# Optimization experiments

Hardware: AMD Instinct MI355X
Metric: run time of the kernel (lower is better)

Reference implementation:

```python
import jax, jax.numpy as jnp
import numpy as np

B, S, H = 128, 512, 512  # batch, seq_len, hidden_units; feature dim is 2H = 1024
D = 2 * H


def setup_inputs() -> dict:
    key = jax.random.key(0)
    ks = jax.random.split(key, 8)
    scale = 1.0 / np.sqrt(D)
    return {
        "h_dec": jax.random.normal(ks[0], (1, B, H), jnp.float32),
        "c_dec": jax.random.normal(ks[1], (1, B, H), jnp.float32),
        "encoder_output": jax.random.normal(ks[2], (B, S, D), jnp.float32),
        "x_padding_masks": jnp.ones((B, S), jnp.float32),
        "coverage_vector": jax.random.uniform(ks[3], (B, S), jnp.float32),
        "Wh_w": jax.random.normal(ks[4], (D, D), jnp.float32) * scale,
        "Ws_w": jax.random.normal(ks[5], (D, D), jnp.float32) * scale,
        "Ws_b": jax.random.normal(ks[6], (D,), jnp.float32) * scale,
        "v_w": jax.random.normal(ks[7], (D,), jnp.float32) * scale,
        "wc_w": jax.random.normal(jax.random.fold_in(key, 99), (D,), jnp.float32) * scale,
    }


def reference(h_dec, c_dec, encoder_output, x_padding_masks, coverage_vector,
              Wh_w, Ws_w, Ws_b, v_w, wc_w):
    # s_t: concat(h, c) -> (B, 2H)
    s_t = jnp.concatenate([h_dec[0], c_dec[0]], axis=-1)  # (B, D)
    enc_feat = jnp.einsum('bsd,ed->bse', encoder_output, Wh_w)       # Wh(enc)
    dec_feat = s_t @ Ws_w.T + Ws_b                                    # (B, D)
    cov_feat = coverage_vector[:, :, None] * wc_w[None, None, :]      # w_c(cov)
    att_inputs = enc_feat + dec_feat[:, None, :] + cov_feat           # (B, S, D)
    score = jnp.tanh(att_inputs) @ v_w                                # (B, S)
    aw = jax.nn.softmax(score, axis=1) * x_padding_masks              # masked softmax
    aw = aw / jnp.sum(aw, axis=1, keepdims=True)                      # renormalize
    context_vector = jnp.einsum('bs,bsd->bd', aw, encoder_output)     # (B, D)
    new_coverage = coverage_vector + aw
    return context_vector, aw, new_coverage
```

## Files before the change

### kernel.cpp

```cpp
#include <hip/hip_runtime.h>
#include <hip/hip_bf16.h>
#include <cstdint>
#include <cstddef>


typedef __attribute__((ext_vector_type(8))) short bf16x8;
typedef __attribute__((ext_vector_type(4))) float f32x4;

#define GLOBAL_AS(p) ((const __attribute__((address_space(1))) unsigned int*)(p))
#define LDS_AS(p)    ((__attribute__((address_space(3))) unsigned int*)(p))

__device__ __forceinline__ short f2bf(float f) {
    union { float f; uint32_t u; } v; v.f = f;
    uint32_t u = v.u + 0x7fffu + ((v.u >> 16) & 1u);
    return (short)(u >> 16);
}

__device__ __forceinline__ float bf2f(short s) {
    union { uint32_t u; float f; } v; v.u = ((uint32_t)(uint16_t)s) << 16;
    return v.f;
}

__device__ __forceinline__ bf16x8 cvt8(float4 a, float4 b) {
    bf16x8 r;
    r[0] = f2bf(a.x); r[1] = f2bf(a.y); r[2] = f2bf(a.z); r[3] = f2bf(a.w);
    r[4] = f2bf(b.x); r[5] = f2bf(b.y); r[6] = f2bf(b.z); r[7] = f2bf(b.w);
    return r;
}

__device__ __forceinline__ float fast_tanh(float x) {
    x = fminf(10.f, fmaxf(-10.f, x));
    float e = __expf(2.f * x);
    return (e - 1.f) / (e + 1.f);
}

__global__ __launch_bounds__(256) void cvt_all(
    const float* __restrict__ enc, const float* __restrict__ Wh,
    short* __restrict__ enc_bf, short* __restrict__ Wh_bf)
{
    size_t i = ((size_t)blockIdx.x * 256 + threadIdx.x) * 8;
    const float* src; short* dst; size_t off;
    const size_t NE = 67108864;
    if (i < NE) { src = enc; dst = enc_bf; off = i; }
    else        { src = Wh;  dst = Wh_bf;  off = i - NE; }
    float4 a = *(const float4*)(src + off);
    float4 b = *(const float4*)(src + off + 4);
    *(bf16x8*)(dst + off) = cvt8(a, b);
}

__global__ void cvt_f32_bf16(const float* __restrict__ src, short* __restrict__ dst, int n) {
    int i = (blockIdx.x * 256 + threadIdx.x) * 4;
    if (i < n) {
        float4 f = *(const float4*)(src + i);
        short4 o;
        o.x = f2bf(f.x); o.y = f2bf(f.y); o.z = f2bf(f.z); o.w = f2bf(f.w);
        *(short4*)(dst + i) = o;
    }
}

__global__ __launch_bounds__(256) void dec_gemm_sk(
    const float* __restrict__ hd, const float* __restrict__ cd,
    const float* __restrict__ Ws, float* __restrict__ dec_part)
{
    __shared__ __align__(16) short As[128 * 40];
    __shared__ __align__(16) short Bs[128 * 40];
    const int t = threadIdx.x;
    const int bx = blockIdx.x & 7;
    const int kc = blockIdx.x >> 3;
    const int wv = t >> 6, lane = t & 63, q = lane >> 4, c = lane & 15;
    const int wm = wv & 1, wn = wv >> 1;
    const int ar = t >> 1, ah = t & 1;

    const float* abase = ((kc < 2) ? hd : cd) + (size_t)ar * 512 + (kc & 1) * 256 + ah * 16;
    const float* bbase = Ws + ((size_t)(bx * 128 + ar)) * 1024 + kc * 256 + ah * 16;
    short* awr = &As[ar * 40 + ah * 16];
    short* bwr = &Bs[ar * 40 + ah * 16];

    f32x4 acc[4][4];
#pragma unroll
    for (int i = 0; i < 4; ++i)
#pragma unroll
        for (int j = 0; j < 4; ++j) acc[i][j] = (f32x4){0.f, 0.f, 0.f, 0.f};

    for (int k0 = 0; k0 < 256; k0 += 32) {
        const float4* ap = (const float4*)(abase + k0);
        const float4* bp = (const float4*)(bbase + k0);
        float4 a0 = ap[0], a1 = ap[1], a2 = ap[2], a3 = ap[3];
        float4 b0 = bp[0], b1 = bp[1], b2 = bp[2], b3 = bp[3];
        *(bf16x8*)awr = cvt8(a0, a1);
        *(bf16x8*)(awr + 8) = cvt8(a2, a3);
        *(bf16x8*)bwr = cvt8(b0, b1);
        *(bf16x8*)(bwr + 8) = cvt8(b2, b3);
        __syncthreads();
        bf16x8 af[4], bf[4];
#pragma unroll
        for (int i = 0; i < 4; ++i) af[i] = *(const bf16x8*)&As[(wm * 64 + i * 16 + c) * 40 + q * 8];
#pragma unroll
        for (int j = 0; j < 4; ++j) bf[j] = *(const bf16x8*)&Bs[(wn * 64 + j * 16 + c) * 40 + q * 8];
#pragma unroll
        for (int i = 0; i < 4; ++i)
#pragma unroll
            for (int j = 0; j < 4; ++j)
                acc[i][j] = __builtin_amdgcn_mfma_f32_16x16x32_bf16(af[i], bf[j], acc[i][j], 0, 0, 0);
        __syncthreads();
    }

    const int n0 = bx * 128 + wn * 64;
    float* dp = dec_part + (size_t)kc * 131072;
#pragma unroll
    for (int i = 0; i < 4; ++i)
#pragma unroll
        for (int rr = 0; rr < 4; ++rr) {
            int bidx = wm * 64 + i * 16 + q * 4 + rr;
#pragma unroll
            for (int j = 0; j < 4; ++j)
                dp[(size_t)bidx * 1024 + n0 + j * 16 + c] = acc[i][j][rr];
        }
}

__global__ __launch_bounds__(256) void attn_score_gemm4(
    const short* __restrict__ encb, const short* __restrict__ Whb,
    const float* __restrict__ dec_part, const float* __restrict__ Wsb,
    const float* __restrict__ cov,
    const float* __restrict__ wc_w, const float* __restrict__ v_w,
    float* __restrict__ p_part)
{
    __shared__ __align__(16) short As[2][128 * 32];
    __shared__ __align__(16) short Bs[2][128 * 32];
    const int t = threadIdx.x;
    const int lin = blockIdx.x;
    const int xcd = lin & 7;
    const int kk  = lin >> 3;
    const int bx  = kk & 7;
    const int by  = xcd * 64 + (kk >> 3);
    const int b   = by >> 2;
    const int s0  = (by & 3) * 128;

    const int wv = t >> 6, lane = t & 63, q = lane >> 4, c = lane & 15;
    const int wm = wv & 1, wn = wv >> 1;

    const int srow = wv * 16 + (lane >> 2);
    const int gg = (lane & 3) ^ ((srow ^ (srow >> 2)) & 3);
    const short* ag0 = encb + ((size_t)(by * 128 + srow)) * 1024 + gg * 8;
    const short* ag1 = ag0 + (size_t)64 * 1024;
    const short* bg0 = Whb + ((size_t)(bx * 128 + srow)) * 1024 + gg * 8;
    const short* bg1 = bg0 + (size_t)64 * 1024;
    const int lo = wv * 512;

    const int qa = (q ^ ((c ^ (c >> 2)) & 3)) * 8;

    f32x4 acc[4][4];
#pragma unroll
    for (int i = 0; i < 4; ++i)
#pragma unroll
        for (int j = 0; j < 4; ++j) acc[i][j] = (f32x4){0.f, 0.f, 0.f, 0.f};

    __builtin_amdgcn_global_load_lds(GLOBAL_AS(ag0), LDS_AS(&As[0][lo]), 16, 0, 0);
    __builtin_amdgcn_global_load_lds(GLOBAL_AS(ag1), LDS_AS(&As[0][2048 + lo]), 16, 0, 0);
    __builtin_amdgcn_global_load_lds(GLOBAL_AS(bg0), LDS_AS(&Bs[0][lo]), 16, 0, 0);
    __builtin_amdgcn_global_load_lds(GLOBAL_AS(bg1), LDS_AS(&Bs[0][2048 + lo]), 16, 0, 0);
    __syncthreads();

    for (int k0 = 0; k0 < 32; ++k0) {
        const int cur = k0 & 1;
        if (k0 < 31) {
            const int nxt = cur ^ 1;
            const int kb = (k0 + 1) * 32;
            __builtin_amdgcn_global_load_lds(GLOBAL_AS(ag0 + kb), LDS_AS(&As[nxt][lo]), 16, 0, 0);
            __builtin_amdgcn_global_load_lds(GLOBAL_AS(ag1 + kb), LDS_AS(&As[nxt][2048 + lo]), 16, 0, 0);
            __builtin_amdgcn_global_load_lds(GLOBAL_AS(bg0 + kb), LDS_AS(&Bs[nxt][lo]), 16, 0, 0);
            __builtin_amdgcn_global_load_lds(GLOBAL_AS(bg1 + kb), LDS_AS(&Bs[nxt][2048 + lo]), 16, 0, 0);
        }
        bf16x8 af[4], bf[4];
#pragma unroll
        for (int i = 0; i < 4; ++i) af[i] = *(const bf16x8*)&As[cur][(wm * 64 + i * 16 + c) * 32 + qa];
#pragma unroll
        for (int j = 0; j < 4; ++j) bf[j] = *(const bf16x8*)&Bs[cur][(wn * 64 + j * 16 + c) * 32 + qa];
#pragma unroll
        for (int i = 0; i < 4; ++i)
#pragma unroll
            for (int j = 0; j < 4; ++j)
                acc[i][j] = __builtin_amdgcn_mfma_f32_16x16x32_bf16(af[i], bf[j], acc[i][j], 0, 0, 0);
        __syncthreads();
    }

    const int n0 = bx * 128 + wn * 64;
    float v_e[4], wc_e[4], dec_e[4];
#pragma unroll
    for (int j = 0; j < 4; ++j) {
        int e = n0 + j * 16 + c;
        v_e[j]  = v_w[e];
        wc_e[j] = wc_w[e];
        float d = Wsb[e];
#pragma unroll
        for (int p = 0; p < 4; ++p) d += dec_part[(size_t)p * 131072 + (size_t)b * 1024 + e];
        dec_e[j] = d;
    }
    const float* covb = cov + (size_t)b * 512;
    float* pp = p_part + ((size_t)(bx * 2 + wn)) * 65536 + (size_t)b * 512;
#pragma unroll
    for (int i = 0; i < 4; ++i)
#pragma unroll
        for (int rr = 0; rr < 4; ++rr) {
            int s = s0 + wm * 64 + i * 16 + q * 4 + rr;
            float cs = covb[s];
            float p = 0.f;
#pragma unroll
            for (int j = 0; j < 4; ++j) {
                float att = acc[i][j][rr] + dec_e[j] + cs * wc_e[j];
                p += v_e[j] * fast_tanh(att);
            }
            p += __shfl_xor(p, 1);
            p += __shfl_xor(p, 2);
            p += __shfl_xor(p, 4);
            p += __shfl_xor(p, 8);
            if (c == 0) pp[s] = p;
        }
}

__global__ __launch_bounds__(256) void attn_score_gemm_fb(
    const float* __restrict__ enc, const short* __restrict__ Wh,
    const float* __restrict__ dec_feat, const float* __restrict__ cov,
    const float* __restrict__ wc_w, const float* __restrict__ v_w,
    float* __restrict__ p_part)
{
    __shared__ __align__(16) short As[128 * 40];
    __shared__ __align__(16) short Bs[128 * 40];
    const int t = threadIdx.x;
    const int bx = blockIdx.x;
    const int by = blockIdx.y;
    const int b  = by >> 2;
    const int s0 = (by & 3) * 128;

    const int wv = t >> 6, lane = t & 63, q = lane >> 4, c = lane & 15;
    const int wm = wv & 1, wn = wv >> 1;
    const int ar = t >> 1, ah = t & 1;

    const float* aptr = enc + ((size_t)(by * 128 + ar)) * 1024 + ah * 16;
    const short* bptr = Wh + ((size_t)(bx * 128 + ar)) * 1024 + ah * 16;
    short* awr = &As[ar * 40 + ah * 16];
    short* bwr = &Bs[ar * 40 + ah * 16];

    f32x4 acc[4][4];
#pragma unroll
    for (int i = 0; i < 4; ++i)
#pragma unroll
        for (int j = 0; j < 4; ++j) acc[i][j] = (f32x4){0.f, 0.f, 0.f, 0.f};

    for (int k0 = 0; k0 < 1024; k0 += 32) {
        const float4* ap = (const float4*)(aptr + k0);
        float4 a0 = ap[0], a1 = ap[1], a2 = ap[2], a3 = ap[3];
        bf16x8 bv0 = *(const bf16x8*)(bptr + k0);
        bf16x8 bv1 = *(const bf16x8*)(bptr + k0 + 8);
        *(bf16x8*)awr = cvt8(a0, a1);
        *(bf16x8*)(awr + 8) = cvt8(a2, a3);
        *(bf16x8*)bwr = bv0;
        *(bf16x8*)(bwr + 8) = bv1;
        __syncthreads();
        bf16x8 af[4], bf[4];
#pragma unroll
        for (int i = 0; i < 4; ++i) af[i] = *(const bf16x8*)&As[(wm * 64 + i * 16 + c) * 40 + q * 8];
#pragma unroll
        for (int j = 0; j < 4; ++j) bf[j] = *(const bf16x8*)&Bs[(wn * 64 + j * 16 + c) * 40 + q * 8];
#pragma unroll
        for (int i = 0; i < 4; ++i)
#pragma unroll
            for (int j = 0; j < 4; ++j)
                acc[i][j] = __builtin_amdgcn_mfma_f32_16x16x32_bf16(af[i], bf[j], acc[i][j], 0, 0, 0);
        __syncthreads();
    }

    const int n0 = bx * 128 + wn * 64;
    float v_e[4], wc_e[4], dec_e[4];
#pragma unroll
    for (int j = 0; j < 4; ++j) {
        int e = n0 + j * 16 + c;
        v_e[j]  = v_w[e];
        wc_e[j] = wc_w[e];
        dec_e[j] = dec_feat[(size_t)b * 1024 + e];
    }
    const float* covb = cov + (size_t)b * 512;
    float* pp = p_part + ((size_t)(bx * 2 + wn)) * 65536 + (size_t)b * 512;
#pragma unroll
    for (int i = 0; i < 4; ++i)
#pragma unroll
        for (int rr = 0; rr < 4; ++rr) {
            int s = s0 + wm * 64 + i * 16 + q * 4 + rr;
            float cs = covb[s];
            float p = 0.f;
#pragma unroll
            for (int j = 0; j < 4; ++j) {
                float att = acc[i][j][rr] + dec_e[j] + cs * wc_e[j];
                p += v_e[j] * fast_tanh(att);
            }
            p += __shfl_xor(p, 1);
            p += __shfl_xor(p, 2);
            p += __shfl_xor(p, 4);
            p += __shfl_xor(p, 8);
            if (c == 0) pp[s] = p;
        }
}

__global__ __launch_bounds__(256) void dec_gemm(
    const float* __restrict__ hd, const float* __restrict__ cd,
    const short* __restrict__ Ws, const float* __restrict__ Wsb,
    float* __restrict__ dec_feat)
{
    __shared__ __align__(16) short As[128 * 40];
    __shared__ __align__(16) short Bs[128 * 40];
    const int t = threadIdx.x;
    const int bx = blockIdx.x;
    const int wv = t >> 6, lane = t & 63, q = lane >> 4, c = lane & 15;
    const int wm = wv & 1, wn = wv >> 1;
    const int ar = t >> 1, ah = t & 1;

    const short* bptr = Ws + ((size_t)(bx * 128 + ar)) * 1024 + ah * 16;
    short* awr = &As[ar * 40 + ah * 16];
    short* bwr = &Bs[ar * 40 + ah * 16];

    f32x4 acc[4][4];
#pragma unroll
    for (int i = 0; i < 4; ++i)
#pragma unroll
        for (int j = 0; j < 4; ++j) acc[i][j] = (f32x4){0.f, 0.f, 0.f, 0.f};

    for (int k0 = 0; k0 < 1024; k0 += 32) {
        const int k = k0 + ah * 16;
        const float* src = (k < 512) ? (hd + (size_t)ar * 512 + k)
                                     : (cd + (size_t)ar * 512 + (k - 512));
        const float4* ap = (const float4*)src;
        float4 a0 = ap[0], a1 = ap[1], a2 = ap[2], a3 = ap[3];
        bf16x8 bv0 = *(const bf16x8*)(bptr + k0);
        bf16x8 bv1 = *(const bf16x8*)(bptr + k0 + 8);
        *(bf16x8*)awr = cvt8(a0, a1);
        *(bf16x8*)(awr + 8) = cvt8(a2, a3);
        *(bf16x8*)bwr = bv0;
        *(bf16x8*)(bwr + 8) = bv1;
        __syncthreads();
        bf16x8 af[4], bf[4];
#pragma unroll
        for (int i = 0; i < 4; ++i) af[i] = *(const bf16x8*)&As[(wm * 64 + i * 16 + c) * 40 + q * 8];
#pragma unroll
        for (int j = 0; j < 4; ++j) bf[j] = *(const bf16x8*)&Bs[(wn * 64 + j * 16 + c) * 40 + q * 8];
#pragma unroll
        for (int i = 0; i < 4; ++i)
#pragma unroll
            for (int j = 0; j < 4; ++j)
                acc[i][j] = __builtin_amdgcn_mfma_f32_16x16x32_bf16(af[i], bf[j], acc[i][j], 0, 0, 0);
        __syncthreads();
    }

    const int n0 = bx * 128 + wn * 64;
    float wsb_e[4];
#pragma unroll
    for (int j = 0; j < 4; ++j) wsb_e[j] = Wsb[n0 + j * 16 + c];
#pragma unroll
    for (int i = 0; i < 4; ++i)
#pragma unroll
        for (int rr = 0; rr < 4; ++rr) {
            int bidx = wm * 64 + i * 16 + q * 4 + rr;
#pragma unroll
            for (int j = 0; j < 4; ++j) {
                int e = n0 + j * 16 + c;
                dec_feat[(size_t)bidx * 1024 + e] = acc[i][j][rr] + wsb_e[j];
            }
        }
}

__global__ __launch_bounds__(512) void softmax_kernel(
    const float* __restrict__ p_part, const float* __restrict__ mask,
    const float* __restrict__ cov, float* __restrict__ aw, float* __restrict__ ncov)
{
    __shared__ float red[8];
    const int b = blockIdx.x, t = threadIdx.x;
    const int w = t >> 6, lane = t & 63;
    const size_t idx = (size_t)b * 512 + t;

    float sc = 0.f;
#pragma unroll
    for (int k = 0; k < 16; ++k) sc += p_part[(size_t)k * 65536 + idx];

    float m = sc;
#pragma unroll
    for (int o = 1; o < 64; o <<= 1) m = fmaxf(m, __shfl_xor(m, o));
    if (lane == 0) red[w] = m;
    __syncthreads();
#pragma unroll
    for (int i = 0; i < 8; ++i) m = fmaxf(m, red[i]);
    __syncthreads();

    float e = __expf(sc - m);
    float s = e;
#pragma unroll
    for (int o = 1; o < 64; o <<= 1) s += __shfl_xor(s, o);
    if (lane == 0) red[w] = s;
    __syncthreads();
    s = 0.f;
#pragma unroll
    for (int i = 0; i < 8; ++i) s += red[i];
    __syncthreads();

    float wv = (e / s) * mask[idx];
    float s2 = wv;
#pragma unroll
    for (int o = 1; o < 64; o <<= 1) s2 += __shfl_xor(s2, o);
    if (lane == 0) red[w] = s2;
    __syncthreads();
    s2 = 0.f;
#pragma unroll
    for (int i = 0; i < 8; ++i) s2 += red[i];

    float awv = wv / s2;
    aw[idx] = awv;
    ncov[idx] = cov[idx] + awv;
}

__global__ __launch_bounds__(256) void context_part(
    const short* __restrict__ encb, const float* __restrict__ aw, float* __restrict__ cpart)
{
    const int sc = blockIdx.x & 7;
    const int b  = blockIdx.x >> 3;
    const int t  = threadIdx.x;
    const int dl = t & 127;
    const int si = t >> 7;
    const short* ebase = encb + ((size_t)(b * 512 + sc * 64 + si)) * 1024 + dl * 8;
    const float* awp = aw + (size_t)b * 512 + sc * 64 + si;
    float acc[8];
#pragma unroll
    for (int i = 0; i < 8; ++i) acc[i] = 0.f;
#pragma unroll 16
    for (int s = 0; s < 64; s += 2) {
        float w = awp[s];
        bf16x8 e = *(const bf16x8*)(ebase + (size_t)s * 1024);
#pragma unroll
        for (int i = 0; i < 8; ++i) acc[i] += w * bf2f(e[i]);
    }
    float* cp = cpart + ((size_t)(sc * 2 + si) * 128 + b) * 1024 + dl * 8;
    *(float4*)(cp)     = (float4){acc[0], acc[1], acc[2], acc[3]};
    *(float4*)(cp + 4) = (float4){acc[4], acc[5], acc[6], acc[7]};
}

__global__ __launch_bounds__(256) void ctx_reduce(
    const float* __restrict__ cpart, float* __restrict__ ctx)
{
    int i = blockIdx.x * 256 + threadIdx.x;
    float s = 0.f;
#pragma unroll
    for (int k = 0; k < 16; ++k) s += cpart[(size_t)k * 131072 + i];
    ctx[i] = s;
}

__global__ __launch_bounds__(256) void context_f32(
    const float* __restrict__ enc, const float* __restrict__ aw, float* __restrict__ ctx)
{
    const int schunk = blockIdx.x;
    const int b = blockIdx.y;
    const int t = threadIdx.x;
    const float* ebase = enc + ((size_t)(b * 512 + schunk * 128)) * 1024 + t * 4;
    const float* awp = aw + (size_t)b * 512 + schunk * 128;
    float ax = 0.f, ay = 0.f, az = 0.f, aww = 0.f;
#pragma unroll 4
    for (int s = 0; s < 128; ++s) {
        float w = awp[s];
        float4 e4 = *(const float4*)(ebase + (size_t)s * 1024);
        ax += w * e4.x; ay += w * e4.y; az += w * e4.z; aww += w * e4.w;
    }
    float* cp = ctx + (size_t)b * 1024 + t * 4;
    atomicAdd(cp + 0, ax);
    atomicAdd(cp + 1, ay);
    atomicAdd(cp + 2, az);
    atomicAdd(cp + 3, aww);
}

extern "C" void kernel_launch(void* const* d_in, const int* in_sizes, int n_in,
                              void* d_out, int out_size, void* d_ws, size_t ws_size,
                              hipStream_t stream) {
    const float* hd   = (const float*)d_in[0];
    const float* cd   = (const float*)d_in[1];
    const float* enc  = (const float*)d_in[2];
    const float* mask = (const float*)d_in[3];
    const float* cov  = (const float*)d_in[4];
    const float* Wh   = (const float*)d_in[5];
    const float* Ws   = (const float*)d_in[6];
    const float* Wsb  = (const float*)d_in[7];
    const float* vw   = (const float*)d_in[8];
    const float* wcw  = (const float*)d_in[9];

    float* out  = (float*)d_out;
    float* ctx  = out;
    float* aw   = out + 131072;
    float* ncov = out + 196608;

    char* ws = (char*)d_ws;
    float* p_part   = (float*)ws;
    float* dec_part = (float*)(ws + (4u << 20));
    short* Wh_bf    = (short*)(ws + (6u << 20));
    short* enc_bf   = (short*)(ws + (8u << 20));
    float* cpart    = (float*)ws;
    const size_t need_big = (8ull << 20) + (128ull << 20);

    if (ws_size >= need_big) {
        cvt_all<<<33280, 256, 0, stream>>>(enc, Wh, enc_bf, Wh_bf);
        dec_gemm_sk<<<32, 256, 0, stream>>>(hd, cd, Ws, dec_part);
        attn_score_gemm4<<<4096, 256, 0, stream>>>(enc_bf, Wh_bf, dec_part, Wsb, cov, wcw, vw, p_part);
        softmax_kernel<<<128, 512, 0, stream>>>(p_part, mask, cov, aw, ncov);
        context_part<<<1024, 256, 0, stream>>>(enc_bf, aw, cpart);
        ctx_reduce<<<512, 256, 0, stream>>>(cpart, ctx);
    } else {
        float* dec_feat = (float*)(ws + (4u << 20));
        short* Wh_bf2   = (short*)(ws + (4u << 20) + (512u << 10));
        short* Ws_bf    = (short*)(ws + (6u << 20) + (512u << 10));
        hipMemsetAsync(ctx, 0, 128 * 1024 * sizeof(float), stream);
        cvt_f32_bf16<<<1024, 256, 0, stream>>>(Wh, Wh_bf2, 1024 * 1024);
        cvt_f32_bf16<<<1024, 256, 0, stream>>>(Ws, Ws_bf, 1024 * 1024);
        dec_gemm<<<8, 256, 0, stream>>>(hd, cd, Ws_bf, Wsb, dec_feat);
        attn_score_gemm_fb<<<dim3(8, 512), 256, 0, stream>>>(enc, Wh_bf2, dec_feat, cov, wcw, vw, p_part);
        softmax_kernel<<<128, 512, 0, stream>>>(p_part, mask, cov, aw, ncov);
        context_f32<<<dim3(4, 128), 256, 0, stream>>>(enc, aw, ctx);
    }
}
```

Measured before the change: 654.0 us.

## Enlarge score GEMM tile to 256x128 and fold dec GEMM into convert kernel

The attention-score GEMM now computes a 256x128 tile per block, with each wave owning 64 rows across all 128 columns. This halves the block count and the number of partial score slices that softmax must sum (16 down to 8), and it raises reuse of each loaded Wh tile. The small decoder GEMM is merged into the bf16 conversion launch as extra trailing blocks, which removes one kernel launch. The trade-off is that per-wave accumulators double to 4x8 MFMA tiles, which raises register pressure, and the kernel is declared with launch bounds for two blocks per CU.

Result: faster. 638.0 us (-2.4%).

```diff
diff --git a/kernel.cpp b/kernel.cpp
--- a/kernel.cpp
+++ b/kernel.cpp
@@ -34,39 +34,31 @@
     return (e - 1.f) / (e + 1.f);
 }
 
-__global__ __launch_bounds__(256) void cvt_all(
+__global__ __launch_bounds__(256) void cvt_plus_dec(
     const float* __restrict__ enc, const float* __restrict__ Wh,
-    short* __restrict__ enc_bf, short* __restrict__ Wh_bf)
-{
-    size_t i = ((size_t)blockIdx.x * 256 + threadIdx.x) * 8;
-    const float* src; short* dst; size_t off;
-    const size_t NE = 67108864;
-    if (i < NE) { src = enc; dst = enc_bf; off = i; }
-    else        { src = Wh;  dst = Wh_bf;  off = i - NE; }
-    float4 a = *(const float4*)(src + off);
-    float4 b = *(const float4*)(src + off + 4);
-    *(bf16x8*)(dst + off) = cvt8(a, b);
-}
-
-__global__ void cvt_f32_bf16(const float* __restrict__ src, short* __restrict__ dst, int n) {
-    int i = (blockIdx.x * 256 + threadIdx.x) * 4;
-    if (i < n) {
-        float4 f = *(const float4*)(src + i);
-        short4 o;
-        o.x = f2bf(f.x); o.y = f2bf(f.y); o.z = f2bf(f.z); o.w = f2bf(f.w);
-        *(short4*)(dst + i) = o;
-    }
-}
-
-__global__ __launch_bounds__(256) void dec_gemm_sk(
+    short* __restrict__ enc_bf, short* __restrict__ Wh_bf,
     const float* __restrict__ hd, const float* __restrict__ cd,
     const float* __restrict__ Ws, float* __restrict__ dec_part)
 {
     __shared__ __align__(16) short As[128 * 40];
     __shared__ __align__(16) short Bs[128 * 40];
     const int t = threadIdx.x;
-    const int bx = blockIdx.x & 7;
-    const int kc = blockIdx.x >> 3;
+
+    if (blockIdx.x < 33280) {
+        size_t i = ((size_t)blockIdx.x * 256 + t) * 8;
+        const float* src; short* dst; size_t off;
+        const size_t NE = 67108864;
+        if (i < NE) { src = enc; dst = enc_bf; off = i; }
+        else        { src = Wh;  dst = Wh_bf;  off = i - NE; }
+        float4 a = *(const float4*)(src + off);
+        float4 b = *(const float4*)(src + off + 4);
+        *(bf16x8*)(dst + off) = cvt8(a, b);
+        return;
+    }
+
+    const int bid = blockIdx.x - 33280;
+    const int bx = bid & 7;
+    const int kc = bid >> 3;
     const int wv = t >> 6, lane = t & 63, q = lane >> 4, c = lane & 15;
     const int wm = wv & 1, wn = wv >> 1;
     const int ar = t >> 1, ah = t & 1;
@@ -118,47 +110,61 @@
         }
 }
 
-__global__ __launch_bounds__(256) void attn_score_gemm4(
+__global__ __launch_bounds__(256, 2) void attn_score_gemm5(
     const short* __restrict__ encb, const short* __restrict__ Whb,
     const float* __restrict__ dec_part, const float* __restrict__ Wsb,
     const float* __restrict__ cov,
     const float* __restrict__ wc_w, const float* __restrict__ v_w,
     float* __restrict__ p_part)
 {
-    __shared__ __align__(16) short As[2][128 * 32];
+    __shared__ __align__(16) short As[2][256 * 32];
     __shared__ __align__(16) short Bs[2][128 * 32];
     const int t = threadIdx.x;
     const int lin = blockIdx.x;
     const int xcd = lin & 7;
     const int kk  = lin >> 3;
     const int bx  = kk & 7;
-    const int by  = xcd * 64 + (kk >> 3);
-    const int b   = by >> 2;
-    const int s0  = (by & 3) * 128;
+    const int my  = xcd * 32 + (kk >> 3);
+    const int m0  = my * 256;
+    const int b   = my >> 1;
+    const int s0  = (my & 1) * 256;
 
     const int wv = t >> 6, lane = t & 63, q = lane >> 4, c = lane & 15;
-    const int wm = wv & 1, wn = wv >> 1;
-
-    const int srow = wv * 16 + (lane >> 2);
-    const int gg = (lane & 3) ^ ((srow ^ (srow >> 2)) & 3);
-    const short* ag0 = encb + ((size_t)(by * 128 + srow)) * 1024 + gg * 8;
-    const short* ag1 = ag0 + (size_t)64 * 1024;
-    const short* bg0 = Whb + ((size_t)(bx * 128 + srow)) * 1024 + gg * 8;
-    const short* bg1 = bg0 + (size_t)64 * 1024;
-    const int lo = wv * 512;
+
+    const int srow4 = lane >> 2;
+    const int gg = (lane & 3) ^ ((srow4 ^ (srow4 >> 2)) & 3);
+
+    const short* ag[4];
+    int loA[4];
+#pragma unroll
+    for (int p = 0; p < 4; ++p) {
+        int row = p * 64 + wv * 16 + srow4;
+        ag[p] = encb + ((size_t)(m0 + row)) * 1024 + gg * 8;
+        loA[p] = (p * 64 + wv * 16) * 32;
+    }
+    const short* bg[2];
+    int loB[2];
+#pragma unroll
+    for (int r = 0; r < 2; ++r) {
+        int row = r * 64 + wv * 16 + srow4;
+        bg[r] = Whb + ((size_t)(bx * 128 + row)) * 1024 + gg * 8;
+        loB[r] = (r * 64 + wv * 16) * 32;
+    }
 
     const int qa = (q ^ ((c ^ (c >> 2)) & 3)) * 8;
 
-    f32x4 acc[4][4];
-#pragma unroll
-    for (int i = 0; i < 4; ++i)
-#pragma unroll
-        for (int j = 0; j < 4; ++j) acc[i][j] = (f32x4){0.f, 0.f, 0.f, 0.f};
-
-    __builtin_amdgcn_global_load_lds(GLOBAL_AS(ag0), LDS_AS(&As[0][lo]), 16, 0, 0);
-    __builtin_amdgcn_global_load_lds(GLOBAL_AS(ag1), LDS_AS(&As[0][2048 + lo]), 16, 0, 0);
-    __builtin_amdgcn_global_load_lds(GLOBAL_AS(bg0), LDS_AS(&Bs[0][lo]), 16, 0, 0);
-    __builtin_amdgcn_global_load_lds(GLOBAL_AS(bg1), LDS_AS(&Bs[0][2048 + lo]), 16, 0, 0);
+    f32x4 acc[4][8];
+#pragma unroll
+    for (int i = 0; i < 4; ++i)
+#pragma unroll
+        for (int j = 0; j < 8; ++j) acc[i][j] = (f32x4){0.f, 0.f, 0.f, 0.f};
+
+#pragma unroll
+    for (int p = 0; p < 4; ++p)
+        __builtin_amdgcn_global_load_lds(GLOBAL_AS(ag[p]), LDS_AS(&As[0][loA[p]]), 16, 0, 0);
+#pragma unroll
+    for (int r = 0; r < 2; ++r)
+        __builtin_amdgcn_global_load_lds(GLOBAL_AS(bg[r]), LDS_AS(&Bs[0][loB[r]]), 16, 0, 0);
     __syncthreads();
 
     for (int k0 = 0; k0 < 32; ++k0) {
@@ -166,28 +172,30 @@
         if (k0 < 31) {
             const int nxt = cur ^ 1;
             const int kb = (k0 + 1) * 32;
-            __builtin_amdgcn_global_load_lds(GLOBAL_AS(ag0 + kb), LDS_AS(&As[nxt][lo]), 16, 0, 0);
-            __builtin_amdgcn_global_load_lds(GLOBAL_AS(ag1 + kb), LDS_AS(&As[nxt][2048 + lo]), 16, 0, 0);
-            __builtin_amdgcn_global_load_lds(GLOBAL_AS(bg0 + kb), LDS_AS(&Bs[nxt][lo]), 16, 0, 0);
-            __builtin_amdgcn_global_load_lds(GLOBAL_AS(bg1 + kb), LDS_AS(&Bs[nxt][2048 + lo]), 16, 0, 0);
+#pragma unroll
+            for (int p = 0; p < 4; ++p)
+                __builtin_amdgcn_global_load_lds(GLOBAL_AS(ag[p] + kb), LDS_AS(&As[nxt][loA[p]]), 16, 0, 0);
+#pragma unroll
+            for (int r = 0; r < 2; ++r)
+                __builtin_amdgcn_global_load_lds(GLOBAL_AS(bg[r] + kb), LDS_AS(&Bs[nxt][loB[r]]), 16, 0, 0);
         }
-        bf16x8 af[4], bf[4];
-#pragma unroll
-        for (int i = 0; i < 4; ++i) af[i] = *(const bf16x8*)&As[cur][(wm * 64 + i * 16 + c) * 32 + qa];
-#pragma unroll
-        for (int j = 0; j < 4; ++j) bf[j] = *(const bf16x8*)&Bs[cur][(wn * 64 + j * 16 + c) * 32 + qa];
+        bf16x8 af[4], bf[8];
+#pragma unroll
+        for (int i = 0; i < 4; ++i) af[i] = *(const bf16x8*)&As[cur][(wv * 64 + i * 16 + c) * 32 + qa];
+#pragma unroll
+        for (int j = 0; j < 8; ++j) bf[j] = *(const bf16x8*)&Bs[cur][(j * 16 + c) * 32 + qa];
 #pragma unroll
         for (int i = 0; i < 4; ++i)
 #pragma unroll
-            for (int j = 0; j < 4; ++j)
+            for (int j = 0; j < 8; ++j)
                 acc[i][j] = __builtin_amdgcn_mfma_f32_16x16x32_bf16(af[i], bf[j], acc[i][j], 0, 0, 0);
         __syncthreads();
     }
 
-    const int n0 = bx * 128 + wn * 64;
-    float v_e[4], wc_e[4], dec_e[4];
-#pragma unroll
-    for (int j = 0; j < 4; ++j) {
+    const int n0 = bx * 128;
+    float v_e[8], wc_e[8], dec_e[8];
+#pragma unroll
+    for (int j = 0; j < 8; ++j) {
         int e = n0 + j * 16 + c;
         v_e[j]  = v_w[e];
         wc_e[j] = wc_w[e];
@@ -197,16 +205,16 @@
         dec_e[j] = d;
     }
     const float* covb = cov + (size_t)b * 512;
-    float* pp = p_part + ((size_t)(bx * 2 + wn)) * 65536 + (size_t)b * 512;
+    float* pp = p_part + (size_t)bx * 65536 + (size_t)b * 512;
 #pragma unroll
     for (int i = 0; i < 4; ++i)
 #pragma unroll
         for (int rr = 0; rr < 4; ++rr) {
-            int s = s0 + wm * 64 + i * 16 + q * 4 + rr;
+            int s = s0 + wv * 64 + i * 16 + q * 4 + rr;
             float cs = covb[s];
             float p = 0.f;
 #pragma unroll
-            for (int j = 0; j < 4; ++j) {
+            for (int j = 0; j < 8; ++j) {
                 float att = acc[i][j][rr] + dec_e[j] + cs * wc_e[j];
                 p += v_e[j] * fast_tanh(att);
             }
@@ -368,7 +376,7 @@
 }
 
 __global__ __launch_bounds__(512) void softmax_kernel(
-    const float* __restrict__ p_part, const float* __restrict__ mask,
+    const float* __restrict__ p_part, int ns, const float* __restrict__ mask,
     const float* __restrict__ cov, float* __restrict__ aw, float* __restrict__ ncov)
 {
     __shared__ float red[8];
@@ -377,8 +385,7 @@
     const size_t idx = (size_t)b * 512 + t;
 
     float sc = 0.f;
-#pragma unroll
-    for (int k = 0; k < 16; ++k) sc += p_part[(size_t)k * 65536 + idx];
+    for (int k = 0; k < ns; ++k) sc += p_part[(size_t)k * 65536 + idx];
 
     float m = sc;
 #pragma unroll
@@ -470,6 +477,16 @@
     atomicAdd(cp + 1, ay);
     atomicAdd(cp + 2, az);
     atomicAdd(cp + 3, aww);
+}
+
+__global__ void cvt_f32_bf16(const float* __restrict__ src, short* __restrict__ dst, int n) {
+    int i = (blockIdx.x * 256 + threadIdx.x) * 4;
+    if (i < n) {
+        float4 f = *(const float4*)(src + i);
+        short4 o;
+        o.x = f2bf(f.x); o.y = f2bf(f.y); o.z = f2bf(f.z); o.w = f2bf(f.w);
+        *(short4*)(dst + i) = o;
+    }
 }
 
 extern "C" void kernel_launch(void* const* d_in, const int* in_sizes, int n_in,
@@ -493,20 +510,20 @@
 
     char* ws = (char*)d_ws;
     float* p_part   = (float*)ws;
-    float* dec_part = (float*)(ws + (4u << 20));
-    short* Wh_bf    = (short*)(ws + (6u << 20));
+    float* dec_part = (float*)(ws + (2u << 20));
+    short* Wh_bf    = (short*)(ws + (4u << 20));
     short* enc_bf   = (short*)(ws + (8u << 20));
     float* cpart    = (float*)ws;
     const size_t need_big = (8ull << 20) + (128ull << 20);
 
     if (ws_size >= need_big) {
-        cvt_all<<<33280, 256, 0, stream>>>(enc, Wh, enc_bf, Wh_bf);
-        dec_gemm_sk<<<32, 256, 0, stream>>>(hd, cd, Ws, dec_part);
-        attn_score_gemm4<<<4096, 256, 0, stream>>>(enc_bf, Wh_bf, dec_part, Wsb, cov, wcw, vw, p_part);
-        softmax_kernel<<<128, 512, 0, stream>>>(p_part, mask, cov, aw, ncov);
+        cvt_plus_dec<<<33312, 256, 0, stream>>>(enc, Wh, enc_bf, Wh_bf, hd, cd, Ws, dec_part);
+        attn_score_gemm5<<<2048, 256, 0, stream>>>(enc_bf, Wh_bf, dec_part, Wsb, cov, wcw, vw, p_part);
+        softmax_kernel<<<128, 512, 0, stream>>>(p_part, 8, mask, cov, aw, ncov);
         context_part<<<1024, 256, 0, stream>>>(enc_bf, aw, cpart);
         ctx_reduce<<<512, 256, 0, stream>>>(cpart, ctx);
     } else {
+        float* p_part16 = (float*)ws;
         float* dec_feat = (float*)(ws + (4u << 20));
         short* Wh_bf2   = (short*)(ws + (4u << 20) + (512u << 10));
         short* Ws_bf    = (short*)(ws + (6u << 20) + (512u << 10));
@@ -514,8 +531,8 @@
         cvt_f32_bf16<<<1024, 256, 0, stream>>>(Wh, Wh_bf2, 1024 * 1024);
         cvt_f32_bf16<<<1024, 256, 0, stream>>>(Ws, Ws_bf, 1024 * 1024);
         dec_gemm<<<8, 256, 0, stream>>>(hd, cd, Ws_bf, Wsb, dec_feat);
-        attn_score_gemm_fb<<<dim3(8, 512), 256, 0, stream>>>(enc, Wh_bf2, dec_feat, cov, wcw, vw, p_part);
-        softmax_kernel<<<128, 512, 0, stream>>>(p_part, mask, cov, aw, ncov);
+        attn_score_gemm_fb<<<dim3(8, 512), 256, 0, stream>>>(enc, Wh_bf2, dec_feat, cov, wcw, vw, p_part16);
+        softmax_kernel<<<128, 512, 0, stream>>>(p_part16, 16, mask, cov, aw, ncov);
         context_f32<<<dim3(4, 128), 256, 0, stream>>>(enc, aw, ctx);
     }
 }
```
